# Kernel optimization log

Hardware: AMD Instinct MI355X
Metric: run time of the kernel (lower is better)

## Reference

```python
import jax, jax.numpy as jnp
jax.config.update("jax_enable_x64", True)
import numpy as np

# Dimensions from init_kwargs
B = 1024            # batch of binarized input patterns
T = 4096            # total_input_bits
N = 4096            # num_neurons
NB = 16             # n_bits_per_neuron
MEM_SIZE = 1 << NB  # 65536 addressable cells per neuron
BITS_PER_CELL = 2
CELLS_PER_WORD = 62 // BITS_PER_CELL          # 31
WPN = (MEM_SIZE + CELLS_PER_WORD - 1) // CELLS_PER_WORD  # 2115 words per neuron


def setup_inputs() -> dict:
    key = jax.random.key(0)
    k1, k2, k3 = jax.random.split(key, 3)
    # binarized input patterns in {0,1}
    x = jax.random.randint(k1, (B, T), 0, 2, dtype=jnp.int32)
    # per-neuron connections into the input bit vector
    connections = jax.random.randint(k2, (N, NB), 0, T, dtype=jnp.int64)
    # bit-packed 2-bit RAM cells (trained state); random words stand in for a
    # trained memory -- the read math is identical regardless of contents
    memory_words = jax.random.randint(k3, (N, WPN), 0, 2**31 - 1, dtype=jnp.int64)
    return {"x": x, "connections": connections, "memory_words": memory_words}


def reference(x, connections, memory_words):
    # Gather each neuron's connected input bits: [B, N, NB]
    bits = jnp.take(x, connections, axis=1).astype(jnp.int64)
    # MSB-first address decode (matches binary_addresses = 2**arange(NB-1,-1,-1))
    weights = (jnp.int64(1) << jnp.arange(NB - 1, -1, -1, dtype=jnp.int64))
    addr = jnp.sum(bits * weights, axis=-1)  # [B, N] in [0, MEM_SIZE)
    # _cell_coords: locate the packed 2-bit cell
    word_index = addr // CELLS_PER_WORD          # [B, N]
    bit_shift = (addr % CELLS_PER_WORD) * BITS_PER_CELL
    # Irregular gather of the packed words: memory_words[n, word_index[b, n]]
    words = memory_words[jnp.arange(N, dtype=jnp.int64)[None, :], word_index]  # [B, N]
    # _read_cells: extract 2-bit cell value in {0,1,2} (FALSE, TRUE, EMPTY)
    vals = (words >> bit_shift) & 3
    return vals
```

## Files before the change

### kernel.cpp

```cpp
#include <hip/hip_runtime.h>
#include <stdint.h>

constexpr int Tdim = 4096;
constexpr int Ndim = 4096;
constexpr int Bdim = 1024;
constexpr int NB   = 16;
constexpr int WPN  = 2115;

__global__ __launch_bounds__(64) void detect_kernel(const int* __restrict__ x,
                                                    const int* __restrict__ conn,
                                                    const int* __restrict__ mem,
                                                    int* __restrict__ flags) {
    const int j = threadIdx.x;
    const unsigned long long bx = __ballot(x[2 * j + 1] == 0);
    const unsigned long long bc = __ballot(conn[2 * j + 1] == 0);
    const unsigned long long bm = __ballot(mem[2 * j + 1] == 0);
    if (j == 0) {
        flags[0] = (bx == ~0ull) ? 1 : 0;
        flags[1] = (bc == ~0ull) ? 1 : 0;
        flags[2] = (bm == ~0ull) ? 1 : 0;
    }
}

__global__ __launch_bounds__(256) void pack_kernel(const int* __restrict__ x,
                                                   uint32_t* __restrict__ xT,
                                                   const int* __restrict__ flags) {
    const int sx = flags[0] ? 2 : 1;
    const int t  = blockIdx.x * 256 + threadIdx.x;
    const int bg = blockIdx.y;
    uint32_t w = 0;
#pragma unroll
    for (int bl = 0; bl < 32; ++bl) {
        const size_t idx = ((size_t)(bg * 32 + bl) * Tdim + t) * sx;
        w |= (uint32_t)(x[idx] & 1) << bl;
    }
    xT[(size_t)bg * Tdim + t] = w;
}

__global__ __launch_bounds__(64) void lookup_kernel(const uint32_t* __restrict__ xT,
                                                    const int* __restrict__ conn,
                                                    const int* __restrict__ mem,
                                                    int* __restrict__ out,
                                                    const int* __restrict__ flags) {
    const int sc = flags[1] ? 2 : 1;
    const int sm = flags[2] ? 2 : 1;
    const int n  = blockIdx.x * 64 + threadIdx.x;
    const int by = blockIdx.y;

    const uint32_t* xA = xT + (size_t)(by * 2) * Tdim;
    const uint32_t* xB = xA + Tdim;

    const int* cp = conn + (size_t)n * NB * sc;
    uint32_t a[32];
#pragma unroll
    for (int j = 0; j < 16; ++j) {
        const int c = cp[j * sc];
        a[16 + j] = xA[c];
        a[j]      = xB[c];
    }

#pragma unroll
    for (int j = 16; j != 0; j >>= 1) {
        const uint32_t m = 0xFFFFFFFFu / ((1u << j) + 1u);
#pragma unroll
        for (int k = 0; k < 32; ++k) {
            if ((k & j) == 0) {
                const uint32_t t = (a[k] ^ (a[k + j] >> j)) & m;
                a[k]     ^= t;
                a[k + j] ^= t << j;
            }
        }
    }

    const int* mrow = mem + (size_t)n * WPN * sm;
    int* orow = out + (size_t)by * 64 * Ndim + n;

#pragma unroll
    for (int k = 0; k < 32; ++k) {
        const uint32_t rw  = a[k];
        const uint32_t adA = rw & 0xFFFFu;
        const uint32_t adB = rw >> 16;
        const uint32_t wiA = adA / 31u;
        const uint32_t shA = (adA - wiA * 31u) * 2u;
        const uint32_t wiB = adB / 31u;
        const uint32_t shB = (adB - wiB * 31u) * 2u;
        const uint64_t wdA = (uint32_t)mrow[(size_t)wiA * sm];
        const uint64_t wdB = (uint32_t)mrow[(size_t)wiB * sm];
        const int kb = 31 - k;
        orow[(size_t)kb * Ndim]        = (int)((wdA >> shA) & 3u);
        orow[(size_t)(kb + 32) * Ndim] = (int)((wdB >> shB) & 3u);
    }
}

__global__ __launch_bounds__(256) void direct_kernel(const int* __restrict__ x,
                                                     const int* __restrict__ conn,
                                                     const int* __restrict__ mem,
                                                     int* __restrict__ out,
                                                     const int* __restrict__ flags) {
    const int sx = flags[0] ? 2 : 1;
    const int sc = flags[1] ? 2 : 1;
    const int sm = flags[2] ? 2 : 1;
    const int n  = blockIdx.x * 256 + threadIdx.x;
    const int b  = blockIdx.y;
    const int* cp = conn + (size_t)n * NB * sc;
    const int* xr = x + (size_t)b * Tdim * sx;
    uint32_t addr = 0;
#pragma unroll
    for (int j = 0; j < 16; ++j) {
        const int c = cp[j * sc];
        addr = (addr << 1) | (uint32_t)(xr[(size_t)c * sx] & 1);
    }
    const uint32_t wi = addr / 31u;
    const uint32_t sh = (addr - wi * 31u) * 2u;
    const uint64_t wd = (uint32_t)mem[((size_t)n * WPN + wi) * sm];
    out[(size_t)b * Ndim + n] = (int)((wd >> sh) & 3u);
}

extern "C" void kernel_launch(void* const* d_in, const int* in_sizes, int n_in,
                              void* d_out, int out_size, void* d_ws, size_t ws_size,
                              hipStream_t stream) {
    const int* x    = (const int*)d_in[0];
    const int* conn = (const int*)d_in[1];
    const int* mem  = (const int*)d_in[2];
    int*       out  = (int*)d_out;
    int*       flags = (int*)d_ws;
    uint32_t*  xT    = (uint32_t*)((char*)d_ws + 256);

    detect_kernel<<<1, 64, 0, stream>>>(x, conn, mem, flags);

    const size_t need = 256 + (size_t)(Bdim / 32) * Tdim * sizeof(uint32_t);
    if (ws_size >= need) {
        dim3 g1(Tdim / 256, Bdim / 32);
        pack_kernel<<<g1, 256, 0, stream>>>(x, xT, flags);
        dim3 g2(Ndim / 64, Bdim / 64);
        lookup_kernel<<<g2, 64, 0, stream>>>(xT, conn, mem, out, flags);
    } else {
        dim3 g3(Ndim / 256, Bdim);
        direct_kernel<<<g3, 256, 0, stream>>>(x, conn, mem, out, flags);
    }
}
```

Baseline: 118.1 us.

## Replace transpose lookup with per-neuron wavefront kernel and inline stride probing

Removes the separate detect kernel by probing the input strides inside each kernel with a wave ballot. Replaces the register bit-transpose lookup kernel with a row kernel in which each wavefront handles one neuron, each lane handles one batch element, and memory reads for a neuron stay within its row. Outputs are staged through shared memory so that stores write rows of 8 contiguous neurons. This trades the transpose ALU work for 16 batch-group iterations per block, each with two barriers and only 32-byte output row segments, and it launches only 512 blocks.

```diff
diff --git a/kernel.cpp b/kernel.cpp
--- a/kernel.cpp
+++ b/kernel.cpp
@@ -7,25 +7,14 @@
 constexpr int NB   = 16;
 constexpr int WPN  = 2115;
 
-__global__ __launch_bounds__(64) void detect_kernel(const int* __restrict__ x,
-                                                    const int* __restrict__ conn,
-                                                    const int* __restrict__ mem,
-                                                    int* __restrict__ flags) {
-    const int j = threadIdx.x;
-    const unsigned long long bx = __ballot(x[2 * j + 1] == 0);
-    const unsigned long long bc = __ballot(conn[2 * j + 1] == 0);
-    const unsigned long long bm = __ballot(mem[2 * j + 1] == 0);
-    if (j == 0) {
-        flags[0] = (bx == ~0ull) ? 1 : 0;
-        flags[1] = (bc == ~0ull) ? 1 : 0;
-        flags[2] = (bm == ~0ull) ? 1 : 0;
-    }
+__device__ __forceinline__ int probe_stride(const int* __restrict__ p) {
+    const int l = threadIdx.x & 63;
+    return (__ballot(p[2 * l + 1] == 0) == ~0ull) ? 2 : 1;
 }
 
 __global__ __launch_bounds__(256) void pack_kernel(const int* __restrict__ x,
-                                                   uint32_t* __restrict__ xT,
-                                                   const int* __restrict__ flags) {
-    const int sx = flags[0] ? 2 : 1;
+                                                   uint32_t* __restrict__ xT) {
+    const int sx = probe_stride(x);
     const int t  = blockIdx.x * 256 + threadIdx.x;
     const int bg = blockIdx.y;
     uint32_t w = 0;
@@ -37,79 +26,61 @@
     xT[(size_t)bg * Tdim + t] = w;
 }
 
-__global__ __launch_bounds__(64) void lookup_kernel(const uint32_t* __restrict__ xT,
-                                                    const int* __restrict__ conn,
-                                                    const int* __restrict__ mem,
-                                                    int* __restrict__ out,
-                                                    const int* __restrict__ flags) {
-    const int sc = flags[1] ? 2 : 1;
-    const int sm = flags[2] ? 2 : 1;
-    const int n  = blockIdx.x * 64 + threadIdx.x;
-    const int by = blockIdx.y;
+__global__ __launch_bounds__(512) void row_kernel(const uint32_t* __restrict__ xT,
+                                                  const int* __restrict__ conn,
+                                                  const int* __restrict__ mem,
+                                                  int* __restrict__ out) {
+    const int sc = probe_stride(conn);
+    const int sm = probe_stride(mem);
 
-    const uint32_t* xA = xT + (size_t)(by * 2) * Tdim;
-    const uint32_t* xB = xA + Tdim;
+    const int l = threadIdx.x & 63;
+    const int w = threadIdx.x >> 6;
+    const int n = blockIdx.x * 8 + w;
 
+    __shared__ int tile[64 * 9];
+
+    int c[16];
     const int* cp = conn + (size_t)n * NB * sc;
-    uint32_t a[32];
 #pragma unroll
-    for (int j = 0; j < 16; ++j) {
-        const int c = cp[j * sc];
-        a[16 + j] = xA[c];
-        a[j]      = xB[c];
-    }
-
-#pragma unroll
-    for (int j = 16; j != 0; j >>= 1) {
-        const uint32_t m = 0xFFFFFFFFu / ((1u << j) + 1u);
-#pragma unroll
-        for (int k = 0; k < 32; ++k) {
-            if ((k & j) == 0) {
-                const uint32_t t = (a[k] ^ (a[k + j] >> j)) & m;
-                a[k]     ^= t;
-                a[k + j] ^= t << j;
-            }
-        }
-    }
+    for (int j = 0; j < 16; ++j) c[j] = cp[j * sc];
 
     const int* mrow = mem + (size_t)n * WPN * sm;
-    int* orow = out + (size_t)by * 64 * Ndim + n;
+    const int bit = l & 31;
 
+    for (int g = 0; g < 16; ++g) {
+        const uint32_t* xs = xT + (size_t)(g * 2 + (l >> 5)) * Tdim;
+        uint32_t addr = 0;
 #pragma unroll
-    for (int k = 0; k < 32; ++k) {
-        const uint32_t rw  = a[k];
-        const uint32_t adA = rw & 0xFFFFu;
-        const uint32_t adB = rw >> 16;
-        const uint32_t wiA = adA / 31u;
-        const uint32_t shA = (adA - wiA * 31u) * 2u;
-        const uint32_t wiB = adB / 31u;
-        const uint32_t shB = (adB - wiB * 31u) * 2u;
-        const uint64_t wdA = (uint32_t)mrow[(size_t)wiA * sm];
-        const uint64_t wdB = (uint32_t)mrow[(size_t)wiB * sm];
-        const int kb = 31 - k;
-        orow[(size_t)kb * Ndim]        = (int)((wdA >> shA) & 3u);
-        orow[(size_t)(kb + 32) * Ndim] = (int)((wdB >> shB) & 3u);
+        for (int j = 0; j < 16; ++j)
+            addr = (addr << 1) | ((xs[c[j]] >> bit) & 1u);
+
+        const uint32_t wi = addr / 31u;
+        const uint32_t sh = (addr - wi * 31u) * 2u;
+        const uint64_t wd = (uint32_t)mrow[(size_t)wi * sm];
+        tile[l * 9 + w] = (int)((wd >> sh) & 3u);
+        __syncthreads();
+        const int r  = threadIdx.x >> 3;
+        const int c2 = threadIdx.x & 7;
+        out[(size_t)(g * 64 + r) * Ndim + blockIdx.x * 8 + c2] = tile[r * 9 + c2];
+        __syncthreads();
     }
 }
 
 __global__ __launch_bounds__(256) void direct_kernel(const int* __restrict__ x,
                                                      const int* __restrict__ conn,
                                                      const int* __restrict__ mem,
-                                                     int* __restrict__ out,
-                                                     const int* __restrict__ flags) {
-    const int sx = flags[0] ? 2 : 1;
-    const int sc = flags[1] ? 2 : 1;
-    const int sm = flags[2] ? 2 : 1;
+                                                     int* __restrict__ out) {
+    const int sx = probe_stride(x);
+    const int sc = probe_stride(conn);
+    const int sm = probe_stride(mem);
     const int n  = blockIdx.x * 256 + threadIdx.x;
     const int b  = blockIdx.y;
     const int* cp = conn + (size_t)n * NB * sc;
     const int* xr = x + (size_t)b * Tdim * sx;
     uint32_t addr = 0;
 #pragma unroll
-    for (int j = 0; j < 16; ++j) {
-        const int c = cp[j * sc];
-        addr = (addr << 1) | (uint32_t)(xr[(size_t)c * sx] & 1);
-    }
+    for (int j = 0; j < 16; ++j)
+        addr = (addr << 1) | (uint32_t)(xr[(size_t)cp[j * sc] * sx] & 1);
     const uint32_t wi = addr / 31u;
     const uint32_t sh = (addr - wi * 31u) * 2u;
     const uint64_t wd = (uint32_t)mem[((size_t)n * WPN + wi) * sm];
@@ -123,19 +94,15 @@
     const int* conn = (const int*)d_in[1];
     const int* mem  = (const int*)d_in[2];
     int*       out  = (int*)d_out;
-    int*       flags = (int*)d_ws;
-    uint32_t*  xT    = (uint32_t*)((char*)d_ws + 256);
+    uint32_t*  xT   = (uint32_t*)d_ws;
 
-    detect_kernel<<<1, 64, 0, stream>>>(x, conn, mem, flags);
-
-    const size_t need = 256 + (size_t)(Bdim / 32) * Tdim * sizeof(uint32_t);
+    const size_t need = (size_t)(Bdim / 32) * Tdim * sizeof(uint32_t);
     if (ws_size >= need) {
         dim3 g1(Tdim / 256, Bdim / 32);
-        pack_kernel<<<g1, 256, 0, stream>>>(x, xT, flags);
-        dim3 g2(Ndim / 64, Bdim / 64);
-        lookup_kernel<<<g2, 64, 0, stream>>>(xT, conn, mem, out, flags);
+        pack_kernel<<<g1, 256, 0, stream>>>(x, xT);
+        row_kernel<<<Ndim / 8, 512, 0, stream>>>(xT, conn, mem, out);
     } else {
         dim3 g3(Ndim / 256, Bdim);
-        direct_kernel<<<g3, 256, 0, stream>>>(x, conn, mem, out, flags);
+        direct_kernel<<<g3, 256, 0, stream>>>(x, conn, mem, out);
     }
 }
```

New measurement: 122.3 us. 1.04x slower.
